# Optimization experiments

Measured on AMD Instinct MI355X. Metric: run time of the kernel, lower is better.

The kernel has to match this reference:

```python
import jax, jax.numpy as jnp
import numpy as np

ROPE_BASE = 1000000.0
EPS = 1e-6
N_HEADS = 8


def apply_rope(x, base=ROPE_BASE):
    # x: [b, s, h, d]
    b, s, h, d = x.shape
    half = d // 2
    theta = 1.0 / base ** (2 * jnp.arange(half) / d)          # [half]
    angles = jnp.arange(s)[:, None] * theta[None, :]          # [s, half]
    cos = jnp.cos(angles)[None, :, None, :]                   # [1, s, 1, half]
    sin = jnp.sin(angles)[None, :, None, :]
    x1, x2 = jnp.split(x, 2, axis=-1)
    return jnp.concatenate([x1 * cos - x2 * sin, x1 * sin + x2 * cos], axis=-1)


def setup_inputs() -> dict:
    key = jax.random.key(0)
    ks = jax.random.split(key, 5)
    b, s, dim = 2, 4096, 512
    x = jax.random.normal(ks[0], (b, s, dim), dtype=jnp.float32)
    scale = jnp.ones((dim,), dtype=jnp.float32)
    init = 1.0 / np.sqrt(dim)
    Wq = jax.random.normal(ks[1], (dim, dim), dtype=jnp.float32) * init
    Wk = jax.random.normal(ks[2], (dim, dim), dtype=jnp.float32) * init
    Wv = jax.random.normal(ks[3], (dim, dim), dtype=jnp.float32) * init
    Wo = jax.random.normal(ks[4], (dim, dim), dtype=jnp.float32) * init
    return {"x": x, "scale": scale, "Wq": Wq, "Wk": Wk, "Wv": Wv, "Wo": Wo}


def reference(x, scale, Wq, Wk, Wv, Wo):
    b, s, dim = x.shape
    h = N_HEADS
    dh = dim // h
    # RMSNorm (use_fast_variance=False path)
    variance = jnp.mean(x ** 2, axis=-1, keepdims=True)
    x_norm = x / jnp.sqrt(variance + EPS) * scale
    # Projections (flax Linear: y = x @ kernel, kernel [in, out])
    q = (x_norm @ Wq).reshape(b, s, h, dh)
    k = (x_norm @ Wk).reshape(b, s, h, dh)
    v = (x_norm @ Wv).reshape(b, s, h, dh)
    q = apply_rope(q)
    k = apply_rope(k)
    scores = jnp.einsum('bthd,bshd->bhts', q, k) / jnp.sqrt(jnp.float32(dh))
    mask = jnp.triu(jnp.full((s, s), -jnp.inf, dtype=jnp.float32), k=1)
    scores = scores + mask[None, None, :, :]
    attn = jax.nn.softmax(scores, axis=-1)
    out = jnp.einsum('bhts,bshd->bthd', attn, v).reshape(b, s, dim)
    return out @ Wo
```

## Files before the change

kernel.cpp:

```cpp
#include <hip/hip_runtime.h>
#include <hip/hip_bf16.h>

typedef _Float16 f16;
typedef _Float16 f16x2 __attribute__((ext_vector_type(2)));
typedef _Float16 f16x4 __attribute__((ext_vector_type(4)));
typedef _Float16 f16x8 __attribute__((ext_vector_type(8)));
typedef float f32x4 __attribute__((ext_vector_type(4)));

#define S_LEN 4096
#define DIM   512
#define NH    8
#define DH    64
#define BATCH 2
#define BHDIM (BATCH*NH)
#define ROWS2 (BHDIM*S_LEN)

#define QSCALE 0.18033688011112042f

__device__ __forceinline__ void gld16(const f16* g, f16* l) {
#if __has_builtin(__builtin_amdgcn_global_load_lds)
  __builtin_amdgcn_global_load_lds((const __attribute__((address_space(1))) void*)g,
                                   (__attribute__((address_space(3))) void*)l, 16, 0, 0);
#else
  *(f16x8*)l = *(const f16x8*)g;
#endif
}

__device__ __forceinline__ float fexp2(float x) {
#if __has_builtin(__builtin_amdgcn_exp2f)
  return __builtin_amdgcn_exp2f(x);
#else
  return exp2f(x);
#endif
}

__device__ __forceinline__ f16x2 pk2(float a, float b) {
#if __has_builtin(__builtin_amdgcn_cvt_pkrtz)
  auto r = __builtin_amdgcn_cvt_pkrtz(a, b);
  f16x2 o; __builtin_memcpy(&o, &r, sizeof(o));
  return o;
#else
  f16x2 r; r[0] = (f16)a; r[1] = (f16)b; return r;
#endif
}

__global__ __launch_bounds__(256) void prep_kernel(
    const float* __restrict__ x, const float* __restrict__ scale,
    const float* __restrict__ Wq, const float* __restrict__ Wk,
    const float* __restrict__ Wv, const float* __restrict__ Wo,
    f16* __restrict__ xn, f16* __restrict__ wt_qkv, f16* __restrict__ wo_t,
    float* __restrict__ ctab, float* __restrict__ stab) {
  int bid = blockIdx.x;
  int tid = threadIdx.x;
  if (bid < 8192) {
    const float* xr = x + (size_t)bid * DIM;
    float2 v = *(const float2*)(xr + tid*2);
    float ss = v.x*v.x + v.y*v.y;
    #pragma unroll
    for (int off = 32; off > 0; off >>= 1) ss += __shfl_down(ss, off);
    __shared__ float red[4];
    if ((tid & 63) == 0) red[tid >> 6] = ss;
    __syncthreads();
    float tot = red[0] + red[1] + red[2] + red[3];
    float inv = rsqrtf(tot * (1.0f/DIM) + 1e-6f);
    float2 s = *(const float2*)(scale + tid*2);
    xn[(size_t)bid*DIM + tid*2+0] = (f16)(v.x*inv*s.x);
    xn[(size_t)bid*DIM + tid*2+1] = (f16)(v.y*inv*s.y);
  } else if (bid < 9216) {
    __shared__ f16 tile[32][33];
    int b2 = bid - 8192;
    int mat = b2 >> 8;
    int rem = b2 & 255;
    int k0 = (rem >> 4) * 32, n0 = (rem & 15) * 32;
    const float* src = (mat == 0) ? Wq : (mat == 1) ? Wk : (mat == 2) ? Wv : Wo;
    f16* dst = (mat < 3) ? (wt_qkv + (size_t)mat*DIM*DIM) : wo_t;
    int tx = tid & 31, ty = tid >> 5;
    #pragma unroll
    for (int i = 0; i < 32; i += 8)
      tile[ty+i][tx] = (f16)src[(size_t)(k0+ty+i)*DIM + n0+tx];
    __syncthreads();
    #pragma unroll
    for (int i = 0; i < 32; i += 8)
      dst[(size_t)(n0+ty+i)*DIM + k0+tx] = tile[tx][ty+i];
  } else {
    int idx = (bid - 9216)*256 + tid;
    int t = idx >> 5, d = idx & 31;
    float theta = exp2f(-(float)d * (19.931568569324174f / 32.0f));
    float sv, cv;
    sincosf((float)t * theta, &sv, &cv);
    ctab[idx] = cv; stab[idx] = sv;
  }
}

__device__ __forceinline__ void gemm128_acc(
    const f16* __restrict__ A, const f16* __restrict__ Bt,
    int m0, int n0, f16* As, f16* Bs, f32x4 (&acc)[4][4]) {
  const int tid = threadIdx.x;
  const int wave = tid >> 6, lane = tid & 63;
  const int l16 = lane & 15, quad = lane >> 4;
  const int mrow = (wave & 1) * 64, ncol = (wave >> 1) * 64;
  const int srow = tid >> 3;
  const int gc = (tid & 7) ^ ((tid >> 3) & 7);

  for (int k0 = 0; k0 < DIM; k0 += 64) {
    if (k0) __syncthreads();
    #pragma unroll
    for (int i = 0; i < 4; i++) {
      gld16(A  + (size_t)(m0 + i*32 + srow)*DIM + k0 + gc*8, As + i*2048 + tid*8);
      gld16(Bt + (size_t)(n0 + i*32 + srow)*DIM + k0 + gc*8, Bs + i*2048 + tid*8);
    }
    __syncthreads();
    #pragma unroll
    for (int kc = 0; kc < 2; kc++) {
      f16x8 a[4], b[4];
      #pragma unroll
      for (int mt = 0; mt < 4; mt++) {
        int row = mrow + mt*16 + l16;
        a[mt] = *(const f16x8*)(As + row*64 + (((quad + 4*kc) ^ (l16 & 7)) * 8));
      }
      #pragma unroll
      for (int nt = 0; nt < 4; nt++) {
        int row = ncol + nt*16 + l16;
        b[nt] = *(const f16x8*)(Bs + row*64 + (((quad + 4*kc) ^ (l16 & 7)) * 8));
      }
      #pragma unroll
      for (int mt = 0; mt < 4; mt++)
        #pragma unroll
        for (int nt = 0; nt < 4; nt++)
          acc[mt][nt] = __builtin_amdgcn_mfma_f32_16x16x32_f16(a[mt], b[nt], acc[mt][nt], 0, 0, 0);
    }
  }
}

__global__ __launch_bounds__(256) void qkv_gemm_kernel(
    const f16* __restrict__ xn, const f16* __restrict__ wt,
    const float* __restrict__ ctab, const float* __restrict__ stab,
    f16* __restrict__ qbuf, f16* __restrict__ kbuf, f16* __restrict__ vt) {
  __shared__ __align__(16) f16 As[128*64], Bs[128*64];
  int m0 = blockIdx.x * 128, n0 = blockIdx.y * 128;
  f32x4 acc[4][4] = {};
  gemm128_acc(xn, wt, m0, n0, As, Bs, acc);

  const int tid = threadIdx.x;
  const int wave = tid >> 6, lane = tid & 63;
  const int l16 = lane & 15, quad = lane >> 4;
  int ncol = n0 + (wave >> 1) * 64;
  int which = ncol >> 9;
  int head = (ncol >> 6) & 7;
  int mbase = m0 + (wave & 1) * 64;

  if (which <= 1) {
    #pragma unroll
    for (int mt = 0; mt < 4; mt++)
      #pragma unroll
      for (int nt = 0; nt < 2; nt++) {
        int d = nt*16 + l16;
        #pragma unroll
        for (int r = 0; r < 4; r++) {
          int t = (mbase + mt*16 + quad*4 + r) & 4095;
          float cv = ctab[t*32 + d], sv = stab[t*32 + d];
          float x1 = acc[mt][nt][r], x2 = acc[mt][nt+2][r];
          acc[mt][nt][r]   = x1*cv - x2*sv;
          acc[mt][nt+2][r] = x1*sv + x2*cv;
        }
      }
  }
  if (which < 2) {
    float osc = (which == 0) ? QSCALE : 1.0f;
    f16* dst = which ? kbuf : qbuf;
    #pragma unroll
    for (int mt = 0; mt < 4; mt++)
      #pragma unroll
      for (int nt = 0; nt < 4; nt++)
        #pragma unroll
        for (int r = 0; r < 4; r++) {
          int m = mbase + mt*16 + quad*4 + r;
          int b = m >> 12, t = m & 4095;
          dst[(((size_t)(b*NH + head))*S_LEN + t)*DH + nt*16 + l16] = (f16)(acc[mt][nt][r]*osc);
        }
  } else {
    #pragma unroll
    for (int mt = 0; mt < 4; mt++)
      #pragma unroll
      for (int nt = 0; nt < 4; nt++) {
        int m = mbase + mt*16 + quad*4;
        int b = m >> 12, tcol = m & 4095;
        int grp = tcol & ~63;
        int pos = ((mt >> 1)*4 + quad)*8 + (mt & 1)*4;
        int d = nt*16 + l16;
        f16x4 v4 = {(f16)acc[mt][nt][0], (f16)acc[mt][nt][1],
                    (f16)acc[mt][nt][2], (f16)acc[mt][nt][3]};
        *(f16x4*)(vt + ((size_t)((b*NH + head)*DH + d))*S_LEN + grp + pos) = v4;
      }
  }
}

__global__ __launch_bounds__(256, 5) void attn_kernel(
    const f16* __restrict__ qbuf, const f16* __restrict__ kbuf,
    const f16* __restrict__ vtb, f16* __restrict__ po,
    float* __restrict__ pm, float* __restrict__ pl) {
  int bid = blockIdx.x;
  int bh  = bid & 15;
  int hf  = (bid >> 4) & 1;
  int p   = bid >> 5;

  int tid = threadIdx.x;
  int wave = tid >> 6, lane = tid & 63;
  int l16 = lane & 15, quad = lane >> 4;
  int bi = wave >> 1, half = wave & 1;

  const f16* Q = qbuf + (size_t)bh*S_LEN*DH;
  const f16* K = kbuf + (size_t)bh*S_LEN*DH;
  const f16* V = vtb  + (size_t)bh*DH*S_LEN;

  int bv = bi ? p : (127 - p);
  int tc = (bv >> 1) + 1;
  int T0 = ((127 - p) >> 1) + 1;
  int nloc = (T0 - hf + 1) >> 1;
  int rbase = bv*32 + half*16;

  f16x8 qa0, qa1;
  {
    const f16* qrow = Q + (size_t)(rbase + l16)*DH + quad*8;
    qa0 = *(const f16x8*)(qrow);
    qa1 = *(const f16x8*)(qrow + 32);
  }

  f32x4 o[4] = {};
  float m_i = -1e30f;
  float l_i = 0.f;

  __shared__ __align__(16) f16 kt[2*4096];
  __shared__ __align__(16) f16 vs[2*4096];

  const int srow = tid >> 3;
  const int gcs = (tid & 7) ^ (srow & 7);

  #define STAGE(buf, kv)                                                        \
    do {                                                                        \
      f16* ktb = kt + (buf)*4096;                                               \
      f16* vsb = vs + (buf)*4096;                                               \
      _Pragma("unroll")                                                         \
      for (int n = 0; n < 2; n++) {                                             \
        gld16(K + (size_t)((kv) + n*32 + srow)*DH + gcs*8, ktb + n*2048 + tid*8);\
        gld16(V + (size_t)(n*32 + srow)*S_LEN + (kv) + gcs*8, vsb + n*2048 + tid*8);\
      }                                                                         \
    } while (0)

  STAGE(0, hf*64);
  __syncthreads();

  for (int itl = 0; itl < nloc; ++itl) {
    int g = 2*itl + hf;
    int kv0 = g * 64;
    int cur = itl & 1;
    if (itl + 1 < nloc) STAGE(cur ^ 1, kv0 + 128);

    const f16* ktc = kt + cur*4096;
    const f16* vsc = vs + cur*4096;

    if (g < tc) {
      bool diag = (g == tc - 1);
      int ntl = diag ? ((bv & 1) ? 4 : 2) : 4;
      int kcl = ntl >> 1;

      f32x4 st[4];
      #pragma unroll
      for (int nt = 0; nt < 4; nt++) {
        if (nt >= ntl) continue;
        int row = nt*16 + l16;
        f16x8 kf0 = *(const f16x8*)(ktc + row*64 + (((quad)     ^ (row & 7))*8));
        f16x8 kf1 = *(const f16x8*)(ktc + row*64 + (((quad + 4) ^ (row & 7))*8));
        f32x4 z = {};
        z = __builtin_amdgcn_mfma_f32_16x16x32_f16(kf0, qa0, z, 0, 0, 0);
        st[nt] = __builtin_amdgcn_mfma_f32_16x16x32_f16(kf1, qa1, z, 0, 0, 0);
      }

      int qglob = rbase + l16;
      float rmx = -1e30f;
      #pragma unroll
      for (int nt = 0; nt < 4; nt++) {
        if (nt >= ntl) continue;
        if (diag) {
          int kb = kv0 + nt*16 + quad*4;
          #pragma unroll
          for (int r = 0; r < 4; r++) {
            float v = st[nt][r];
            if (kb + r > qglob) v = -1e30f;
            st[nt][r] = v;
            rmx = fmaxf(rmx, v);
          }
        } else {
          #pragma unroll
          for (int r = 0; r < 4; r++) rmx = fmaxf(rmx, st[nt][r]);
        }
      }
      rmx = fmaxf(rmx, __shfl_xor(rmx, 16));
      rmx = fmaxf(rmx, __shfl_xor(rmx, 32));
      if (!__all(rmx <= m_i + 8.0f)) {
        float mnew = fmaxf(m_i, rmx);
        float alpha = fexp2(m_i - mnew);
        m_i = mnew;
        float al[4];
        #pragma unroll
        for (int r = 0; r < 4; r++) al[r] = __shfl(alpha, quad*4 + r);
        #pragma unroll
        for (int dnt = 0; dnt < 4; dnt++)
          #pragma unroll
          for (int r = 0; r < 4; r++) o[dnt][r] *= al[r];
        l_i *= alpha;
      }
      float mref = m_i;
      float rs = 0.f;
      f16x8 pa[2];
      #pragma unroll
      for (int c = 0; c < 2; c++) {
        if (c >= kcl) continue;
        float e0 = fexp2(st[2*c  ][0] - mref);
        float e1 = fexp2(st[2*c  ][1] - mref);
        float e2 = fexp2(st[2*c  ][2] - mref);
        float e3 = fexp2(st[2*c  ][3] - mref);
        float e4 = fexp2(st[2*c+1][0] - mref);
        float e5 = fexp2(st[2*c+1][1] - mref);
        float e6 = fexp2(st[2*c+1][2] - mref);
        float e7 = fexp2(st[2*c+1][3] - mref);
        rs += ((e0+e1)+(e2+e3)) + ((e4+e5)+(e6+e7));
        f16x4 h0 = __builtin_shufflevector(pk2(e0,e1), pk2(e2,e3), 0,1,2,3);
        f16x4 h1 = __builtin_shufflevector(pk2(e4,e5), pk2(e6,e7), 0,1,2,3);
        pa[c] = __builtin_shufflevector(h0, h1, 0,1,2,3,4,5,6,7);
      }
      l_i += rs;

      #pragma unroll
      for (int c = 0; c < 2; c++) {
        if (c >= kcl) continue;
        #pragma unroll
        for (int dnt = 0; dnt < 4; dnt++) {
          int vr = dnt*16 + l16;
          f16x8 vf = *(const f16x8*)(vsc + vr*64 + (((c*4 + quad) ^ (vr & 7))*8));
          o[dnt] = __builtin_amdgcn_mfma_f32_16x16x32_f16(pa[c], vf, o[dnt], 0, 0, 0);
        }
      }
    }

    __syncthreads();
  }
  #undef STAGE

  {
    float lf = l_i;
    lf += __shfl_xor(lf, 16);
    lf += __shfl_xor(lf, 32);
    if (quad == 0) {
      int t = rbase + l16;
      pm[(size_t)(hf*BHDIM + bh)*S_LEN + t] = m_i;
      pl[(size_t)(hf*BHDIM + bh)*S_LEN + t] = lf;
    }
    float lr[4];
    #pragma unroll
    for (int r = 0; r < 4; r++) lr[r] = __shfl(lf, quad*4 + r);
    #pragma unroll
    for (int r = 0; r < 4; r++) {
      float invl = (lr[r] > 0.f) ? 1.0f / lr[r] : 0.f;
      int t = rbase + quad*4 + r;
      size_t rowoff = ((size_t)(hf*BHDIM + bh)*S_LEN + t)*DH;
      #pragma unroll
      for (int dnt = 0; dnt < 4; dnt++)
        po[rowoff + dnt*16 + l16] = (f16)(o[dnt][r]*invl);
    }
  }
}

__global__ __launch_bounds__(256) void merge_kernel(
    const f16* __restrict__ po, const float* __restrict__ pm,
    const float* __restrict__ pl, f16* __restrict__ ao) {
  int idx = blockIdx.x*256 + threadIdx.x;
  int r_ = idx >> 2, q = idx & 3;
  int bh = r_ >> 12, t = r_ & 4095;
  float m0 = pm[r_], m1 = pm[ROWS2 + r_];
  float l0 = pl[r_], l1 = pl[ROWS2 + r_];
  float M  = fmaxf(m0, m1);
  float a0 = l0 * fexp2(m0 - M);
  float a1 = l1 * fexp2(m1 - M);
  float inv = 1.0f / (a0 + a1);
  float w0 = a0 * inv, w1 = a1 * inv;
  const f16* p0 = po + (size_t)r_*DH + q*16;
  const f16* p1 = po + (size_t)(ROWS2 + r_)*DH + q*16;
  int b = bh >> 3, h = bh & 7;
  f16* dst = ao + ((size_t)(b*S_LEN + t))*DIM + h*DH + q*16;
  f16x8 v0a = *(const f16x8*)(p0), v0b = *(const f16x8*)(p0 + 8);
  f16x8 v1a = *(const f16x8*)(p1), v1b = *(const f16x8*)(p1 + 8);
  f16x8 oa, ob;
  #pragma unroll
  for (int j = 0; j < 8; j++) {
    oa[j] = (f16)(w0*(float)v0a[j] + w1*(float)v1a[j]);
    ob[j] = (f16)(w0*(float)v0b[j] + w1*(float)v1b[j]);
  }
  *(f16x8*)dst = oa;
  *(f16x8*)(dst + 8) = ob;
}

__global__ __launch_bounds__(256) void out_gemm_kernel(
    const f16* __restrict__ ao, const f16* __restrict__ wot,
    float* __restrict__ out) {
  __shared__ __align__(16) f16 As[128*64], Bs[128*64];
  int m0 = blockIdx.x * 128, n0 = blockIdx.y * 128;
  f32x4 acc[4][4] = {};
  gemm128_acc(ao, wot, m0, n0, As, Bs, acc);

  const int tid = threadIdx.x;
  const int wave = tid >> 6, lane = tid & 63;
  const int l16 = lane & 15, quad = lane >> 4;
  int ncol = n0 + (wave >> 1) * 64;
  int mbase = m0 + (wave & 1) * 64;
  #pragma unroll
  for (int mt = 0; mt < 4; mt++)
    #pragma unroll
    for (int nt = 0; nt < 4; nt++)
      #pragma unroll
      for (int r = 0; r < 4; r++)
        out[(size_t)(mbase + mt*16 + quad*4 + r)*DIM + ncol + nt*16 + l16] = acc[mt][nt][r];
}

extern "C" void kernel_launch(void* const* d_in, const int* in_sizes, int n_in,
                              void* d_out, int out_size, void* d_ws, size_t ws_size,
                              hipStream_t stream) {
  const float* x     = (const float*)d_in[0];
  const float* scale = (const float*)d_in[1];
  const float* Wq    = (const float*)d_in[2];
  const float* Wk    = (const float*)d_in[3];
  const float* Wv    = (const float*)d_in[4];
  const float* Wo    = (const float*)d_in[5];
  float* out = (float*)d_out;

  const size_t ROWS = (size_t)BATCH * S_LEN;
  char* ws = (char*)d_ws;
  f16* xn     = (f16*)ws;  ws += ROWS * DIM * sizeof(f16);
  f16* wt_qkv = (f16*)ws;  ws += (size_t)3 * DIM * DIM * sizeof(f16);
  f16* wo_t   = (f16*)ws;  ws += (size_t)DIM * DIM * sizeof(f16);
  f16* qb     = (f16*)ws;  ws += (size_t)BHDIM * S_LEN * DH * sizeof(f16);
  f16* kb     = (f16*)ws;  ws += (size_t)BHDIM * S_LEN * DH * sizeof(f16);
  f16* vt     = (f16*)ws;  ws += (size_t)BHDIM * S_LEN * DH * sizeof(f16);
  float* ctab = (float*)ws; ws += (size_t)S_LEN * 32 * sizeof(float);
  float* stab = (float*)ws; ws += (size_t)S_LEN * 32 * sizeof(float);
  f16* po     = (f16*)ws;  ws += (size_t)2 * ROWS2 * DH * sizeof(f16);
  float* pm   = (float*)ws; ws += (size_t)2 * ROWS2 * sizeof(float);
  float* pl   = (float*)ws; ws += (size_t)2 * ROWS2 * sizeof(float);
  f16* ao     = xn;

  size_t need = (size_t)(ws - (char*)d_ws);
  if (ws_size < need) return;

  prep_kernel    <<<9728, 256, 0, stream>>>(x, scale, Wq, Wk, Wv, Wo,
                                            xn, wt_qkv, wo_t, ctab, stab);
  qkv_gemm_kernel<<<dim3(64,12), 256, 0, stream>>>(xn, wt_qkv, ctab, stab, qb, kb, vt);
  attn_kernel    <<<2048, 256, 0, stream>>>(qb, kb, vt, po, pm, pl);
  merge_kernel   <<<1024, 256, 0, stream>>>(po, pm, pl, ao);
  out_gemm_kernel<<<dim3(64,4), 256, 0, stream>>>(ao, wo_t, out);
}
```

Measured before the change: 189.4 us.

## Fuse split-KV merge into output GEMM and compute row sums via MFMA

Removes the separate merge kernel: the out-projection GEMM now loads both partial attention outputs plus their max/sum statistics and combines them while staging the A tile into shared memory. The attention kernel writes partials directly in [b,t,h*dh] layout so the GEMM can read them contiguously. The softmax row sum is accumulated with an extra MFMA against a ones vector instead of scalar adds and shuffles. This saves one launch and a round trip of the merged activation through memory. In exchange the A tile is loaded synchronously rather than via async LDS loads, and the merge statistics are recomputed by every N-block of the GEMM.

```diff
diff --git a/kernel.cpp b/kernel.cpp
--- a/kernel.cpp
+++ b/kernel.cpp
@@ -227,8 +227,11 @@
   }
 
   f32x4 o[4] = {};
+  f32x4 l_acc = {};
   float m_i = -1e30f;
-  float l_i = 0.f;
+
+  const f16x8 vone = {(f16)1.f,(f16)1.f,(f16)1.f,(f16)1.f,
+                      (f16)1.f,(f16)1.f,(f16)1.f,(f16)1.f};
 
   __shared__ __align__(16) f16 kt[2*4096];
   __shared__ __align__(16) f16 vs[2*4096];
@@ -308,10 +311,10 @@
         for (int dnt = 0; dnt < 4; dnt++)
           #pragma unroll
           for (int r = 0; r < 4; r++) o[dnt][r] *= al[r];
-        l_i *= alpha;
+        #pragma unroll
+        for (int r = 0; r < 4; r++) l_acc[r] *= al[r];
       }
       float mref = m_i;
-      float rs = 0.f;
       f16x8 pa[2];
       #pragma unroll
       for (int c = 0; c < 2; c++) {
@@ -324,12 +327,10 @@
         float e5 = fexp2(st[2*c+1][1] - mref);
         float e6 = fexp2(st[2*c+1][2] - mref);
         float e7 = fexp2(st[2*c+1][3] - mref);
-        rs += ((e0+e1)+(e2+e3)) + ((e4+e5)+(e6+e7));
         f16x4 h0 = __builtin_shufflevector(pk2(e0,e1), pk2(e2,e3), 0,1,2,3);
         f16x4 h1 = __builtin_shufflevector(pk2(e4,e5), pk2(e6,e7), 0,1,2,3);
         pa[c] = __builtin_shufflevector(h0, h1, 0,1,2,3,4,5,6,7);
       }
-      l_i += rs;
 
       #pragma unroll
       for (int c = 0; c < 2; c++) {
@@ -340,6 +341,7 @@
           f16x8 vf = *(const f16x8*)(vsc + vr*64 + (((c*4 + quad) ^ (vr & 7))*8));
           o[dnt] = __builtin_amdgcn_mfma_f32_16x16x32_f16(pa[c], vf, o[dnt], 0, 0, 0);
         }
+        l_acc = __builtin_amdgcn_mfma_f32_16x16x32_f16(pa[c], vone, l_acc, 0, 0, 0);
       }
     }
 
@@ -348,22 +350,24 @@
   #undef STAGE
 
   {
-    float lf = l_i;
-    lf += __shfl_xor(lf, 16);
-    lf += __shfl_xor(lf, 32);
-    if (quad == 0) {
-      int t = rbase + l16;
-      pm[(size_t)(hf*BHDIM + bh)*S_LEN + t] = m_i;
-      pl[(size_t)(hf*BHDIM + bh)*S_LEN + t] = lf;
-    }
-    float lr[4];
-    #pragma unroll
-    for (int r = 0; r < 4; r++) lr[r] = __shfl(lf, quad*4 + r);
+    float mrow[4];
+    #pragma unroll
+    for (int r = 0; r < 4; r++) mrow[r] = __shfl(m_i, quad*4 + r);
+    if (l16 == 0) {
+      #pragma unroll
+      for (int r = 0; r < 4; r++) {
+        int t = rbase + quad*4 + r;
+        pm[(size_t)(hf*BHDIM + bh)*S_LEN + t] = mrow[r];
+        pl[(size_t)(hf*BHDIM + bh)*S_LEN + t] = l_acc[r];
+      }
+    }
+    int b = bh >> 3, h = bh & 7;
     #pragma unroll
     for (int r = 0; r < 4; r++) {
-      float invl = (lr[r] > 0.f) ? 1.0f / lr[r] : 0.f;
+      float invl = (l_acc[r] > 0.f) ? 1.0f / l_acc[r] : 0.f;
       int t = rbase + quad*4 + r;
-      size_t rowoff = ((size_t)(hf*BHDIM + bh)*S_LEN + t)*DH;
+      size_t rowoff = (size_t)hf*(BATCH*S_LEN)*DIM
+                    + ((size_t)(b*S_LEN + t))*DIM + h*DH;
       #pragma unroll
       for (int dnt = 0; dnt < 4; dnt++)
         po[rowoff + dnt*16 + l16] = (f16)(o[dnt][r]*invl);
@@ -371,47 +375,70 @@
   }
 }
 
-__global__ __launch_bounds__(256) void merge_kernel(
+__global__ __launch_bounds__(256) void out_gemm_kernel(
     const f16* __restrict__ po, const float* __restrict__ pm,
-    const float* __restrict__ pl, f16* __restrict__ ao) {
-  int idx = blockIdx.x*256 + threadIdx.x;
-  int r_ = idx >> 2, q = idx & 3;
-  int bh = r_ >> 12, t = r_ & 4095;
-  float m0 = pm[r_], m1 = pm[ROWS2 + r_];
-  float l0 = pl[r_], l1 = pl[ROWS2 + r_];
-  float M  = fmaxf(m0, m1);
-  float a0 = l0 * fexp2(m0 - M);
-  float a1 = l1 * fexp2(m1 - M);
-  float inv = 1.0f / (a0 + a1);
-  float w0 = a0 * inv, w1 = a1 * inv;
-  const f16* p0 = po + (size_t)r_*DH + q*16;
-  const f16* p1 = po + (size_t)(ROWS2 + r_)*DH + q*16;
-  int b = bh >> 3, h = bh & 7;
-  f16* dst = ao + ((size_t)(b*S_LEN + t))*DIM + h*DH + q*16;
-  f16x8 v0a = *(const f16x8*)(p0), v0b = *(const f16x8*)(p0 + 8);
-  f16x8 v1a = *(const f16x8*)(p1), v1b = *(const f16x8*)(p1 + 8);
-  f16x8 oa, ob;
-  #pragma unroll
-  for (int j = 0; j < 8; j++) {
-    oa[j] = (f16)(w0*(float)v0a[j] + w1*(float)v1a[j]);
-    ob[j] = (f16)(w0*(float)v0b[j] + w1*(float)v1b[j]);
-  }
-  *(f16x8*)dst = oa;
-  *(f16x8*)(dst + 8) = ob;
-}
-
-__global__ __launch_bounds__(256) void out_gemm_kernel(
-    const f16* __restrict__ ao, const f16* __restrict__ wot,
+    const float* __restrict__ pl, const f16* __restrict__ wot,
     float* __restrict__ out) {
   __shared__ __align__(16) f16 As[128*64], Bs[128*64];
   int m0 = blockIdx.x * 128, n0 = blockIdx.y * 128;
-  f32x4 acc[4][4] = {};
-  gemm128_acc(ao, wot, m0, n0, As, Bs, acc);
-
   const int tid = threadIdx.x;
   const int wave = tid >> 6, lane = tid & 63;
   const int l16 = lane & 15, quad = lane >> 4;
-  int ncol = n0 + (wave >> 1) * 64;
+  const int mrow = (wave & 1) * 64, ncol = (wave >> 1) * 64;
+  const int srow = tid >> 3;
+  const int gc = (tid & 7) ^ ((tid >> 3) & 7);
+  f32x4 acc[4][4] = {};
+
+  for (int k0 = 0; k0 < DIM; k0 += 64) {
+    if (k0) __syncthreads();
+    int h = k0 >> 6;
+    #pragma unroll
+    for (int i = 0; i < 4; i++)
+      gld16(wot + (size_t)(n0 + i*32 + srow)*DIM + k0 + gc*8, Bs + i*2048 + tid*8);
+    #pragma unroll
+    for (int i = 0; i < 4; i++) {
+      int m = m0 + i*32 + srow;
+      int b = m >> 12, t = m & 4095;
+      int rr = (b*NH + h)*S_LEN + t;
+      float m0v = pm[rr], m1v = pm[ROWS2 + rr];
+      float l0v = pl[rr], l1v = pl[ROWS2 + rr];
+      float M  = fmaxf(m0v, m1v);
+      float a0 = l0v * fexp2(m0v - M);
+      float a1 = l1v * fexp2(m1v - M);
+      float inv = 1.0f / (a0 + a1);
+      float w0 = a0 * inv, w1 = a1 * inv;
+      const f16* p0 = po + (size_t)m*DIM + k0 + gc*8;
+      f16x8 v0 = *(const f16x8*)(p0);
+      f16x8 v1 = *(const f16x8*)(p0 + (size_t)(BATCH*S_LEN)*DIM);
+      f16x8 va;
+      #pragma unroll
+      for (int j = 0; j < 8; j++)
+        va[j] = (f16)(w0*(float)v0[j] + w1*(float)v1[j]);
+      *(f16x8*)(As + i*2048 + tid*8) = va;
+    }
+    __syncthreads();
+    #pragma unroll
+    for (int kc = 0; kc < 2; kc++) {
+      f16x8 a[4], b[4];
+      #pragma unroll
+      for (int mt = 0; mt < 4; mt++) {
+        int row = mrow + mt*16 + l16;
+        a[mt] = *(const f16x8*)(As + row*64 + (((quad + 4*kc) ^ (l16 & 7)) * 8));
+      }
+      #pragma unroll
+      for (int nt = 0; nt < 4; nt++) {
+        int row = ncol + nt*16 + l16;
+        b[nt] = *(const f16x8*)(Bs + row*64 + (((quad + 4*kc) ^ (l16 & 7)) * 8));
+      }
+      #pragma unroll
+      for (int mt = 0; mt < 4; mt++)
+        #pragma unroll
+        for (int nt = 0; nt < 4; nt++)
+          acc[mt][nt] = __builtin_amdgcn_mfma_f32_16x16x32_f16(a[mt], b[nt], acc[mt][nt], 0, 0, 0);
+    }
+  }
+
+  int ncolg = n0 + (wave >> 1) * 64;
   int mbase = m0 + (wave & 1) * 64;
   #pragma unroll
   for (int mt = 0; mt < 4; mt++)
@@ -419,7 +446,7 @@
     for (int nt = 0; nt < 4; nt++)
       #pragma unroll
       for (int r = 0; r < 4; r++)
-        out[(size_t)(mbase + mt*16 + quad*4 + r)*DIM + ncol + nt*16 + l16] = acc[mt][nt][r];
+        out[(size_t)(mbase + mt*16 + quad*4 + r)*DIM + ncolg + nt*16 + l16] = acc[mt][nt][r];
 }
 
 extern "C" void kernel_launch(void* const* d_in, const int* in_sizes, int n_in,
@@ -443,10 +470,9 @@
   f16* vt     = (f16*)ws;  ws += (size_t)BHDIM * S_LEN * DH * sizeof(f16);
   float* ctab = (float*)ws; ws += (size_t)S_LEN * 32 * sizeof(float);
   float* stab = (float*)ws; ws += (size_t)S_LEN * 32 * sizeof(float);
-  f16* po     = (f16*)ws;  ws += (size_t)2 * ROWS2 * DH * sizeof(f16);
+  f16* po     = (f16*)ws;  ws += (size_t)2 * ROWS * DIM * sizeof(f16);
   float* pm   = (float*)ws; ws += (size_t)2 * ROWS2 * sizeof(float);
   float* pl   = (float*)ws; ws += (size_t)2 * ROWS2 * sizeof(float);
-  f16* ao     = xn;
 
   size_t need = (size_t)(ws - (char*)d_ws);
   if (ws_size < need) return;
@@ -455,6 +481,5 @@
                                             xn, wt_qkv, wo_t, ctab, stab);
   qkv_gemm_kernel<<<dim3(64,12), 256, 0, stream>>>(xn, wt_qkv, ctab, stab, qb, kb, vt);
   attn_kernel    <<<2048, 256, 0, stream>>>(qb, kb, vt, po, pm, pl);
-  merge_kernel   <<<1024, 256, 0, stream>>>(po, pm, pl, ao);
-  out_gemm_kernel<<<dim3(64,4), 256, 0, stream>>>(ao, wo_t, out);
-}
+  out_gemm_kernel<<<dim3(64,4), 256, 0, stream>>>(po, pm, pl, wo_t, out);
+}
```

New measurement: 194.9 us. 2.9% more time.
